# Performance work log

Measured on AMD Instinct MI355X. Metric: run time of the kernel, lower is better.

Reference implementation:

```python
import jax, jax.numpy as jnp
import numpy as np

B, T, I, H, O = 16384, 512, 3, 32, 1

def setup_inputs() -> dict:
    key = jax.random.key(0)
    ks = jax.random.split(key, 7)
    s_ih = 1.0 / np.sqrt(H)
    return {
        "x": jax.random.normal(ks[0], (B, T, I), dtype=jnp.float32),
        # PyTorch LSTM params, gate order (i, f, g, o)
        "W_ih": jax.random.uniform(ks[1], (4 * H, I), jnp.float32, -s_ih, s_ih),
        "W_hh": jax.random.uniform(ks[2], (4 * H, H), jnp.float32, -s_ih, s_ih),
        "b_ih": jax.random.uniform(ks[3], (4 * H,), jnp.float32, -s_ih, s_ih),
        "b_hh": jax.random.uniform(ks[4], (4 * H,), jnp.float32, -s_ih, s_ih),
        "W_fc": jax.random.uniform(ks[5], (O, H), jnp.float32, -s_ih, s_ih),
        "b_fc": jax.random.uniform(ks[6], (O,), jnp.float32, -s_ih, s_ih),
    }

def _lstm_last_hidden(x, W_ih, W_hh, b_ih, b_hh):
    # Precompute input projections for all timesteps: [B, T, 4H]
    x_gates = jnp.einsum("bti,gi->btg", x, W_ih) + (b_ih + b_hh)

    def step(carry, xg_t):
        h, c = carry
        gates = xg_t + h @ W_hh.T  # [B, 4H]
        i_g, f_g, g_g, o_g = jnp.split(gates, 4, axis=-1)
        i_g = jax.nn.sigmoid(i_g)
        f_g = jax.nn.sigmoid(f_g)
        g_g = jnp.tanh(g_g)
        o_g = jax.nn.sigmoid(o_g)
        c = f_g * c + i_g * g_g
        h = o_g * jnp.tanh(c)
        return (h, c), None

    h0 = jnp.zeros((x.shape[0], W_hh.shape[1]), dtype=x.dtype)
    c0 = jnp.zeros_like(h0)
    # scan over time: xg time-major [T, B, 4H]
    (hT, _), _ = jax.lax.scan(step, (h0, c0), jnp.swapaxes(x_gates, 0, 1))
    return hT

def reference(x, W_ih, W_hh, b_ih, b_hh, W_fc, b_fc):
    hT = _lstm_last_hidden(x, W_ih, W_hh, b_ih, b_hh)  # [B, H]
    out = hT @ W_fc.T + b_fc  # [B, O]
    return jax.nn.sigmoid(out)
```

## Files before the change

### kernel.cpp

```cpp
#include <hip/hip_runtime.h>
#include <hip/hip_bf16.h>

typedef short bf16x8 __attribute__((ext_vector_type(8)));
typedef float f32x4 __attribute__((ext_vector_type(4)));
typedef unsigned int u32x4 __attribute__((ext_vector_type(4)));

#define MFMA(a, b, c) __builtin_amdgcn_mfma_f32_16x16x32_bf16((a), (b), (c), 0, 0, 0)

__device__ __forceinline__ unsigned short f2bf(float f) {
    unsigned u = __builtin_bit_cast(unsigned, f);
    unsigned r = u + 0x7FFFu + ((u >> 16) & 1u);
    return (unsigned short)(r >> 16);
}

__device__ __forceinline__ unsigned pk_bf16(float lo, float hi) {
    __hip_bfloat162 p = __float22bfloat162_rn(make_float2(lo, hi));
    unsigned r;
    __builtin_memcpy(&r, &p, sizeof(r));
    return r;
}

__device__ __forceinline__ float sigm(float x) {
    float e = __builtin_amdgcn_exp2f(-1.44269504088896f * x);
    return __builtin_amdgcn_rcpf(1.0f + e);
}

__global__ __launch_bounds__(256, 1) void lstm_mfma3_kernel(
    const float* __restrict__ x,
    const float* __restrict__ W_ih,
    const float* __restrict__ W_hh,
    const float* __restrict__ b_ih,
    const float* __restrict__ b_hh,
    const float* __restrict__ W_fc,
    const float* __restrict__ b_fc,
    float* __restrict__ out,
    int n_groups)
{
    const int lane  = threadIdx.x & 63;
    const int wid   = threadIdx.x >> 6;
    const int group = blockIdx.x * 4 + wid;
    if (group >= n_groups) return;

    const int n = lane & 15;
    const int q = lane >> 4;

    const float NL2E  = -1.4426950408889634f;
    const float P2L2E =  2.8853900817779268f;

    bf16x8 A_hh[8], A_x[8];
#pragma unroll
    for (int t = 0; t < 8; ++t) {
        const int g = 16 * t + n;
        const float s = (t == 4 || t == 5) ? P2L2E : NL2E;
        bf16x8 a, ax;
#pragma unroll
        for (int j = 0; j < 8; ++j) {
            const int k = 16 * (j >> 2) + 4 * q + (j & 3);
            a[j] = (short)f2bf(s * W_hh[g * 32 + k]);
            float axv = 0.0f;
            if (q == 0 && j < 4) {
                axv = (j < 3) ? s * W_ih[g * 3 + j] : s * (b_ih[g] + b_hh[g]);
            }
            ax[j] = (short)f2bf(axv);
        }
        A_hh[t] = a;
        A_x[t]  = ax;
    }

    const long bn = (long)group * 16 + n;
    const float4* xv = (const float4*)(x + bn * (512L * 3));

    float cs[8] = {0.f, 0.f, 0.f, 0.f, 0.f, 0.f, 0.f, 0.f};
    float h[8]  = {0.f, 0.f, 0.f, 0.f, 0.f, 0.f, 0.f, 0.f};
    bf16x8 Bh = {0, 0, 0, 0, 0, 0, 0, 0};

    float4 xa = xv[0], xb = xv[1], xc = xv[2];

#define STEP(X0, X1, X2)                                                        \
    do {                                                                        \
        unsigned bx01 = pk_bf16((X0), (X1));                                    \
        unsigned bx23 = pk_bf16((X2), 1.0f);                                    \
        u32x4 bxv = {bx01, bx23, bx01, bx23};                                   \
        bf16x8 Bx = __builtin_bit_cast(bf16x8, bxv);                            \
        f32x4 acc[8];                                                           \
        _Pragma("unroll")                                                       \
        for (int tt = 0; tt < 8; ++tt) {                                        \
            f32x4 z = {0.f, 0.f, 0.f, 0.f};                                     \
            acc[tt] = MFMA(A_x[tt], Bx, z);                                     \
        }                                                                       \
        _Pragma("unroll")                                                       \
        for (int tt = 0; tt < 8; ++tt) acc[tt] = MFMA(A_hh[tt], Bh, acc[tt]);   \
        _Pragma("unroll")                                                       \
        for (int r = 0; r < 4; ++r) {                                           \
            float ei0 = __builtin_amdgcn_exp2f(acc[0][r]);                      \
            float ef0 = __builtin_amdgcn_exp2f(acc[2][r]);                      \
            float eg0 = __builtin_amdgcn_exp2f(acc[4][r]);                      \
            float eo0 = __builtin_amdgcn_exp2f(acc[6][r]);                      \
            float ei1 = __builtin_amdgcn_exp2f(acc[1][r]);                      \
            float ef1 = __builtin_amdgcn_exp2f(acc[3][r]);                      \
            float eg1 = __builtin_amdgcn_exp2f(acc[5][r]);                      \
            float eo1 = __builtin_amdgcn_exp2f(acc[7][r]);                      \
            float ig0 = __builtin_amdgcn_rcpf(1.0f + ei0);                      \
            float fg0 = __builtin_amdgcn_rcpf(1.0f + ef0);                      \
            float rg0 = __builtin_amdgcn_rcpf(1.0f + eg0);                      \
            float og0 = __builtin_amdgcn_rcpf(1.0f + eo0);                      \
            float ig1 = __builtin_amdgcn_rcpf(1.0f + ei1);                      \
            float fg1 = __builtin_amdgcn_rcpf(1.0f + ef1);                      \
            float rg1 = __builtin_amdgcn_rcpf(1.0f + eg1);                      \
            float og1 = __builtin_amdgcn_rcpf(1.0f + eo1);                      \
            float gp0 = fmaf(-5.7707801635558536f, rg0, P2L2E);                 \
            float gp1 = fmaf(-5.7707801635558536f, rg1, P2L2E);                 \
            cs[r]     = fmaf(fg0, cs[r],     ig0 * gp0);                        \
            cs[4 + r] = fmaf(fg1, cs[4 + r], ig1 * gp1);                        \
            float ec0 = __builtin_amdgcn_exp2f(cs[r]);                          \
            float ec1 = __builtin_amdgcn_exp2f(cs[4 + r]);                      \
            float tc0 = fmaf(-2.0f, __builtin_amdgcn_rcpf(1.0f + ec0), 1.0f);   \
            float tc1 = fmaf(-2.0f, __builtin_amdgcn_rcpf(1.0f + ec1), 1.0f);   \
            h[r]      = og0 * tc0;                                              \
            h[4 + r]  = og1 * tc1;                                              \
        }                                                                       \
        u32x4 bhv = {pk_bf16(h[0], h[1]), pk_bf16(h[2], h[3]),                  \
                     pk_bf16(h[4], h[5]), pk_bf16(h[6], h[7])};                 \
        Bh = __builtin_bit_cast(bf16x8, bhv);                                   \
    } while (0)

    for (int w4 = 0; w4 < 128; ++w4) {
        const int nw = (w4 < 127) ? (w4 + 1) : 127;
        float4 na = xv[3 * nw + 0];
        float4 nb = xv[3 * nw + 1];
        float4 nc = xv[3 * nw + 2];

        STEP(xa.x, xa.y, xa.z);
        STEP(xa.w, xb.x, xb.y);
        STEP(xb.z, xb.w, xc.x);
        STEP(xc.y, xc.z, xc.w);

        xa = na; xb = nb; xc = nc;
    }
#undef STEP

    float part = 0.f;
#pragma unroll
    for (int r = 0; r < 4; ++r) {
        part += W_fc[4 * q + r] * h[r];
        part += W_fc[16 + 4 * q + r] * h[4 + r];
    }
    part += __shfl_xor(part, 16, 64);
    part += __shfl_xor(part, 32, 64);
    if (q == 0) {
        out[bn] = sigm(part + b_fc[0]);
    }
}

extern "C" void kernel_launch(void* const* d_in, const int* in_sizes, int n_in,
                              void* d_out, int out_size, void* d_ws, size_t ws_size,
                              hipStream_t stream) {
    const float* x    = (const float*)d_in[0];
    const float* W_ih = (const float*)d_in[1];
    const float* W_hh = (const float*)d_in[2];
    const float* b_ih = (const float*)d_in[3];
    const float* b_hh = (const float*)d_in[4];
    const float* W_fc = (const float*)d_in[5];
    const float* b_fc = (const float*)d_in[6];
    float* out        = (float*)d_out;

    const int n_groups = out_size / 16;
    const int n_blocks = (n_groups + 3) / 4;

    hipLaunchKernelGGL(lstm_mfma3_kernel, dim3(n_blocks), dim3(256), 0, stream,
                       x, W_ih, W_hh, b_ih, b_hh, W_fc, b_fc, out, n_groups);
}
```

Baseline: 332.8 us.

## Pipeline next-step input MFMA and pair gate reciprocals

```diff
diff --git a/kernel.cpp b/kernel.cpp
--- a/kernel.cpp
+++ b/kernel.cpp
@@ -25,7 +25,7 @@
     return __builtin_amdgcn_rcpf(1.0f + e);
 }
 
-__global__ __launch_bounds__(256, 1) void lstm_mfma3_kernel(
+__global__ __launch_bounds__(256, 1) void lstm_mfma5_kernel(
     const float* __restrict__ x,
     const float* __restrict__ W_ih,
     const float* __restrict__ W_hh,
@@ -76,20 +76,33 @@
 
     float4 xa = xv[0], xb = xv[1], xc = xv[2];
 
-#define STEP(X0, X1, X2)                                                        \
+    f32x4 accx[8];
+    {
+        unsigned bx01 = pk_bf16(xa.x, xa.y);
+        unsigned bx23 = pk_bf16(xa.z, 1.0f);
+        u32x4 bxv = {bx01, bx23, bx01, bx23};
+        bf16x8 Bx = __builtin_bit_cast(bf16x8, bxv);
+#pragma unroll
+        for (int tt = 0; tt < 8; ++tt) {
+            f32x4 z = {0.f, 0.f, 0.f, 0.f};
+            accx[tt] = MFMA(A_x[tt], Bx, z);
+        }
+    }
+
+#define STEP(XN0, XN1, XN2)                                                     \
     do {                                                                        \
-        unsigned bx01 = pk_bf16((X0), (X1));                                    \
-        unsigned bx23 = pk_bf16((X2), 1.0f);                                    \
+        f32x4 acc[8];                                                           \
+        _Pragma("unroll")                                                       \
+        for (int tt = 0; tt < 8; ++tt) acc[tt] = MFMA(A_hh[tt], Bh, accx[tt]);  \
+        unsigned bx01 = pk_bf16((XN0), (XN1));                                  \
+        unsigned bx23 = pk_bf16((XN2), 1.0f);                                   \
         u32x4 bxv = {bx01, bx23, bx01, bx23};                                   \
         bf16x8 Bx = __builtin_bit_cast(bf16x8, bxv);                            \
-        f32x4 acc[8];                                                           \
         _Pragma("unroll")                                                       \
         for (int tt = 0; tt < 8; ++tt) {                                        \
             f32x4 z = {0.f, 0.f, 0.f, 0.f};                                     \
-            acc[tt] = MFMA(A_x[tt], Bx, z);                                     \
+            accx[tt] = MFMA(A_x[tt], Bx, z);                                    \
         }                                                                       \
-        _Pragma("unroll")                                                       \
-        for (int tt = 0; tt < 8; ++tt) acc[tt] = MFMA(A_hh[tt], Bh, acc[tt]);   \
         _Pragma("unroll")                                                       \
         for (int r = 0; r < 4; ++r) {                                           \
             float ei0 = __builtin_amdgcn_exp2f(acc[0][r]);                      \
@@ -100,14 +113,18 @@
             float ef1 = __builtin_amdgcn_exp2f(acc[3][r]);                      \
             float eg1 = __builtin_amdgcn_exp2f(acc[5][r]);                      \
             float eo1 = __builtin_amdgcn_exp2f(acc[7][r]);                      \
-            float ig0 = __builtin_amdgcn_rcpf(1.0f + ei0);                      \
-            float fg0 = __builtin_amdgcn_rcpf(1.0f + ef0);                      \
-            float rg0 = __builtin_amdgcn_rcpf(1.0f + eg0);                      \
-            float og0 = __builtin_amdgcn_rcpf(1.0f + eo0);                      \
-            float ig1 = __builtin_amdgcn_rcpf(1.0f + ei1);                      \
-            float fg1 = __builtin_amdgcn_rcpf(1.0f + ef1);                      \
-            float rg1 = __builtin_amdgcn_rcpf(1.0f + eg1);                      \
-            float og1 = __builtin_amdgcn_rcpf(1.0f + eo1);                      \
+            float a0 = 1.0f + ei0, b0 = 1.0f + ef0;                             \
+            float c0 = 1.0f + eg0, d0 = 1.0f + eo0;                             \
+            float a1 = 1.0f + ei1, b1 = 1.0f + ef1;                             \
+            float c1 = 1.0f + eg1, d1 = 1.0f + eo1;                             \
+            float rp0 = __builtin_amdgcn_rcpf(a0 * b0);                         \
+            float rq0 = __builtin_amdgcn_rcpf(c0 * d0);                         \
+            float rp1 = __builtin_amdgcn_rcpf(a1 * b1);                         \
+            float rq1 = __builtin_amdgcn_rcpf(c1 * d1);                         \
+            float ig0 = b0 * rp0, fg0 = a0 * rp0;                               \
+            float rg0 = d0 * rq0, og0 = c0 * rq0;                               \
+            float ig1 = b1 * rp1, fg1 = a1 * rp1;                               \
+            float rg1 = d1 * rq1, og1 = c1 * rq1;                               \
             float gp0 = fmaf(-5.7707801635558536f, rg0, P2L2E);                 \
             float gp1 = fmaf(-5.7707801635558536f, rg1, P2L2E);                 \
             cs[r]     = fmaf(fg0, cs[r],     ig0 * gp0);                        \
@@ -130,10 +147,10 @@
         float4 nb = xv[3 * nw + 1];
         float4 nc = xv[3 * nw + 2];
 
-        STEP(xa.x, xa.y, xa.z);
         STEP(xa.w, xb.x, xb.y);
         STEP(xb.z, xb.w, xc.x);
         STEP(xc.y, xc.z, xc.w);
+        STEP(na.x, na.y, na.z);
 
         xa = na; xb = nb; xc = nc;
     }
@@ -167,6 +184,6 @@
     const int n_groups = out_size / 16;
     const int n_blocks = (n_groups + 3) / 4;
 
-    hipLaunchKernelGGL(lstm_mfma3_kernel, dim3(n_blocks), dim3(256), 0, stream,
+    hipLaunchKernelGGL(lstm_mfma5_kernel, dim3(n_blocks), dim3(256), 0, stream,
                        x, W_ih, W_hh, b_ih, b_hh, W_fc, b_fc, out, n_groups);
 }
```

Result: faster. 317.8 us (-4.5%).
